# Optimization experiments

Measured on AMD Instinct MI355X. Metric: run time of the kernel, lower is better.

The kernel has to match this reference:

```python
import math
import jax, jax.numpy as jnp
import numpy as np

N_HEADS = 16
HIDDEN = 1024
FACTOR = 256
N_DK = HIDDEN // N_HEADS
B, S = 4, 2048


def _linear_params(key, fan_in, fan_out):
    kw, kb = jax.random.split(key)
    bound = 1.0 / math.sqrt(fan_in)
    W = jax.random.uniform(kw, (fan_in, fan_out), jnp.float32, -bound, bound)
    b = jax.random.uniform(kb, (fan_out,), jnp.float32, -bound, bound)
    return W, b


def setup_inputs() -> dict:
    key = jax.random.key(0)
    ks = jax.random.split(key, 12)
    inp = {
        "query": jax.random.normal(ks[0], (B, S, HIDDEN), jnp.float32),
        "key": jax.random.normal(ks[1], (B, S, HIDDEN), jnp.float32),
        "value": jax.random.normal(ks[2], (B, S, HIDDEN), jnp.float32),
        "mask": jax.random.randint(ks[3], (B, S), 0, 2, jnp.int32),
    }
    names = [("pq", HIDDEN, FACTOR), ("tq", FACTOR, HIDDEN),
             ("pk", HIDDEN, FACTOR), ("tk", FACTOR, HIDDEN),
             ("pv", HIDDEN, FACTOR), ("tv", FACTOR, HIDDEN),
             ("po", HIDDEN, FACTOR), ("to", FACTOR, HIDDEN)]
    for i, (nm, fi, fo) in enumerate(names):
        W, b = _linear_params(ks[4 + i], fi, fo)
        inp[f"W{nm}"], inp[f"b{nm}"] = W, b
    return inp


def _factored(x, Wp, bp, Wt, bt):
    # proj -> leaky_relu(0.2) -> tran
    h = jax.nn.leaky_relu(x @ Wp + bp, negative_slope=0.2)
    return h @ Wt + bt


def reference(query, key, value, mask,
              Wpq, bpq, Wtq, btq, Wpk, bpk, Wtk, btk,
              Wpv, bpv, Wtv, btv, Wpo, bpo, Wto, bto):
    bsize = query.shape[0]

    def split_heads(x):  # [B,S,H*Dk] -> [B,H,S,Dk]
        return x.reshape(bsize, -1, N_HEADS, N_DK).transpose(0, 2, 1, 3)

    q = split_heads(_factored(query, Wpq, bpq, Wtq, btq))
    k = split_heads(_factored(key, Wpk, bpk, Wtk, btk))
    v = split_heads(_factored(value, Wpv, bpv, Wtv, btv))

    scores = jnp.einsum("bhqd,bhkd->bhqk", q, k) / math.sqrt(N_DK)
    m = (mask == 0)[:, None, None, :]  # [B,1,1,S]
    scores = jnp.where(m, jnp.float32(-1e20), scores)
    attn = jax.nn.softmax(scores, axis=-1)
    cv = jnp.einsum("bhqk,bhkd->bhqd", attn, v)
    cv = cv.transpose(0, 2, 1, 3).reshape(bsize, -1, N_HEADS * N_DK)
    # dropout omitted (eval mode / deterministic reference)
    return _factored(cv, Wpo, bpo, Wto, bto)
```

## Files before the change

### kernel.cpp

```cpp
#include <hip/hip_runtime.h>
#include <cstdint>
#include <cstddef>

typedef __bf16 bf16_t;
typedef __bf16 bf16x8 __attribute__((ext_vector_type(8)));
typedef float  f32x4  __attribute__((ext_vector_type(4)));
typedef unsigned int uint32x4 __attribute__((ext_vector_type(4)));
typedef unsigned int uint32x2 __attribute__((ext_vector_type(2)));

#define DEV_INLINE __device__ __forceinline__

constexpr int Bsz = 4, Ssz = 2048, HID = 1024, FAC = 256, NH = 16, DKc = 64;
constexpr int Mrows = Bsz * Ssz;
constexpr float QSCALE = 0.18033688011112042f;

struct Ptr8 { const float* p[8]; };
struct Ptr3 { const float* p[3]; };

DEV_INLINE float fast_exp2(float x) {
#if __has_builtin(__builtin_amdgcn_exp2f)
  return __builtin_amdgcn_exp2f(x);
#else
  return exp2f(x);
#endif
}

DEV_INLINE void async16(const void* g, void* l) {
  __builtin_amdgcn_global_load_lds((const __attribute__((address_space(1))) void*)g,
                                   (__attribute__((address_space(3))) void*)l, 16, 0, 0);
}

#define WBAR(N) do { \
  asm volatile("s_waitcnt vmcnt(" #N ") lgkmcnt(0)" ::: "memory"); \
  __builtin_amdgcn_s_barrier(); \
} while (0)

DEV_INLINE int SW(int r) { return (r & 3) | ((r >> 1) & 4); }

__global__ __launch_bounds__(256) void k_prep(Ptr8 w, Ptr8 bsrc, const int* __restrict__ mask,
                                              bf16_t* wpt, bf16_t* wtt,
                                              float* bp, float* bt, float* mf, bf16_t* mb) {
  const int z = blockIdx.z;
  if (z == 8) {
    const int bid = blockIdx.y * 32 + blockIdx.x;
    if (bid >= 64) return;
    const int i = bid * 256 + threadIdx.x;
    if (i < 4 * FAC) bp[i] = bsrc.p[i >> 8][i & 255];
    if (i < 4 * HID) bt[i] = bsrc.p[4 + (i >> 10)][i & 1023];
    if (i < Bsz * Ssz) {
      const float m = (mask[i] != 0) ? 1.f : 0.f;
      mf[i] = m;
      mb[i] = (bf16_t)m;
    }
    return;
  }
  const int K = (z < 4) ? HID : FAC;
  const int N = (z < 4) ? FAC : HID;
  if ((int)(blockIdx.x * 32) >= N || (int)(blockIdx.y * 32) >= K) return;
  __shared__ float t[32][33];
  const float* src = w.p[z];
  bf16_t* dst = (z < 4) ? (wpt + (size_t)z * FAC * HID) : (wtt + (size_t)(z - 4) * FAC * HID);
  const int tx = threadIdx.x & 31, ty = threadIdx.x >> 5;
  const int kb = blockIdx.y * 32, nb = blockIdx.x * 32;
#pragma unroll
  for (int j = 0; j < 4; ++j)
    t[ty + j * 8][tx] = src[(size_t)(kb + ty + j * 8) * N + nb + tx];
  __syncthreads();
#pragma unroll
  for (int j = 0; j < 4; ++j)
    dst[(size_t)(nb + ty + j * 8) * K + kb + tx] = (bf16_t)t[tx][ty + j * 8];
}

__global__ __launch_bounds__(256, 3) void k_gemmP2(Ptr3 Asrc,
                                                   const bf16_t* __restrict__ Bt_,
                                                   const float* __restrict__ biasAll,
                                                   bf16_t* __restrict__ Call) {
  __shared__ __align__(16) bf16_t As[3][64 * 40];
  __shared__ __align__(16) bf16_t Bs[4][128 * 32];

  const int z = blockIdx.z;
  const bf16_t* Bt = Bt_ + (size_t)z * FAC * HID;
  const float* bias = biasAll + z * FAC;
  bf16_t* C = Call + (size_t)z * Mrows * FAC;

  const int tid = threadIdx.x;
  const int lane = tid & 63, wave = tid >> 6;
  const int quad = lane >> 4, l16 = lane & 15;
  const int m0 = blockIdx.y * 64, n0 = blockIdx.x * 128;

  const int brow = wave * 16 + (lane >> 2), bkc = (lane & 3) * 8;
  const bf16_t* gB0 = Bt + (size_t)(n0 + brow) * HID + bkc;
  const bf16_t* gB1 = gB0 + (size_t)64 * HID;

  const int crow = tid >> 2, chalf = (tid & 3) * 8;
  const float* gAf = Asrc.p[z] + (size_t)(m0 + crow) * HID + chalf;

#define ASYNCB(t, buf)                                \
  do {                                                \
    const int k0_ = (t) * 32;                         \
    async16(gB0 + k0_, Bs[buf] + wave * 512);         \
    async16(gB1 + k0_, Bs[buf] + 2048 + wave * 512);  \
  } while (0)

  {
    f32x4 pa = *(const f32x4*)gAf;
    f32x4 pb = *(const f32x4*)(gAf + 4);
    __builtin_amdgcn_sched_barrier(0);
    ASYNCB(0, 0);
    ASYNCB(1, 1);
    union { bf16_t h[8]; uint32x4 u; } o;
#pragma unroll
    for (int j = 0; j < 4; ++j) { o.h[j] = (bf16_t)pa[j]; o.h[4 + j] = (bf16_t)pb[j]; }
    *(uint32x4*)(As[0] + crow * 40 + chalf) = o.u;
  }

  f32x4 acc[4][2] = {};
  constexpr int nk = 32;

  for (int it = 0; it < nk; ++it) {
    f32x4 xa, xb;
    const int k1 = (it + 1) * 32;
    if (it + 1 < nk) {
      xa = *(const f32x4*)(gAf + k1);
      xb = *(const f32x4*)(gAf + k1 + 4);
    }
    __builtin_amdgcn_sched_barrier(0);
    if (it + 2 < nk) ASYNCB(it + 2, (it + 2) & 3);

    if (it + 2 < nk)      WBAR(6);
    else if (it + 1 < nk) WBAR(4);
    else                  WBAR(0);

    const bf16_t* Ac = As[it % 3];
    const bf16_t* Bc = Bs[it & 3];
    bf16x8 af[4], bfr[2];
#pragma unroll
    for (int i = 0; i < 4; ++i)
      af[i] = *(const bf16x8*)(Ac + (i * 16 + l16) * 40 + quad * 8);
#pragma unroll
    for (int i = 0; i < 2; ++i)
      bfr[i] = *(const bf16x8*)(Bc + (wave * 32 + i * 16 + l16) * 32 + quad * 8);
#pragma unroll
    for (int mi = 0; mi < 4; ++mi)
#pragma unroll
      for (int ni = 0; ni < 2; ++ni)
        acc[mi][ni] = __builtin_amdgcn_mfma_f32_16x16x32_bf16(af[mi], bfr[ni], acc[mi][ni], 0, 0, 0);

    if (it + 1 < nk) {
      union { bf16_t h[8]; uint32x4 u; } o;
#pragma unroll
      for (int j = 0; j < 4; ++j) { o.h[j] = (bf16_t)xa[j]; o.h[4 + j] = (bf16_t)xb[j]; }
      *(uint32x4*)(As[(it + 1) % 3] + crow * 40 + chalf) = o.u;
    }
  }
#undef ASYNCB

#pragma unroll
  for (int mi = 0; mi < 4; ++mi) {
    const int rbase = m0 + mi * 16 + quad * 4;
#pragma unroll
    for (int ni = 0; ni < 2; ++ni) {
      const int col = n0 + wave * 32 + ni * 16 + l16;
      const float bv = bias[col];
#pragma unroll
      for (int r = 0; r < 4; ++r) {
        float y = acc[mi][ni][r] + bv;
        y = (y > 0.f) ? y : 0.2f * y;
        C[(size_t)(rbase + r) * FAC + col] = (bf16_t)y;
      }
    }
  }
}

template <int EPI, typename OUT_T>
__global__ __launch_bounds__(256, 2) void k_gemmQ(const bf16_t* __restrict__ Aall,
                                                  const bf16_t* __restrict__ Btall,
                                                  const float* __restrict__ biasAll,
                                                  OUT_T* __restrict__ Call,
                                                  bf16_t* __restrict__ C2,
                                                  const float* __restrict__ rowmul,
                                                  int N, int K,
                                                  long long Az, long long Bz, long long Cz, int biasz) {
  __shared__ __align__(16) bf16_t As[5][128 * 32];
  __shared__ __align__(16) bf16_t Bs[5][128 * 32];

  const int z = blockIdx.z;
  const bf16_t* Bt = Btall + (size_t)z * Bz;
  const float* bias = biasAll + (size_t)z * biasz;
  OUT_T* C = Call + (size_t)z * Cz;

  const int tid = threadIdx.x;
  const int lane = tid & 63, wave = tid >> 6;
  const int quad = lane >> 4, l16 = lane & 15;
  const int wr = wave >> 1, wc = wave & 1;
  const int m0 = blockIdx.y * 128, n0 = blockIdx.x * 128;

  const int arow = wave * 16 + (lane >> 2), akc = (lane & 3) * 8;
  const bf16_t* gB0 = Bt + (size_t)(n0 + arow) * K + akc;
  const bf16_t* gB1 = gB0 + (size_t)64 * K;
  const bf16_t* A = Aall + (size_t)z * Az;
  const bf16_t* gA0 = A + (size_t)(m0 + arow) * K + akc;
  const bf16_t* gA1 = gA0 + (size_t)64 * K;

#define STAGEQ(t, buf)                               \
  do {                                               \
    const int k0_ = (t) * 32;                        \
    async16(gA0 + k0_, As[buf] + wave * 512);        \
    async16(gA1 + k0_, As[buf] + 2048 + wave * 512); \
    async16(gB0 + k0_, Bs[buf] + wave * 512);        \
    async16(gB1 + k0_, Bs[buf] + 2048 + wave * 512); \
  } while (0)

  const int nk = K / 32;
  STAGEQ(0, 0);
  STAGEQ(1, 1);
  STAGEQ(2, 2);

  f32x4 acc[4][4] = {};

  for (int it = 0; it < nk; ++it) {
    if (it + 3 < nk) STAGEQ(it + 3, (it + 3) % 5);

    if (it + 3 < nk)      WBAR(12);
    else if (it + 2 < nk) WBAR(8);
    else if (it + 1 < nk) WBAR(4);
    else                  WBAR(0);

    const bf16_t* Ac = As[it % 5];
    const bf16_t* Bc = Bs[it % 5];
    bf16x8 af[4], bfr[4];
#pragma unroll
    for (int i = 0; i < 4; ++i)
      af[i] = *(const bf16x8*)(Ac + (wr * 64 + i * 16 + l16) * 32 + quad * 8);
#pragma unroll
    for (int i = 0; i < 4; ++i)
      bfr[i] = *(const bf16x8*)(Bc + (wc * 64 + i * 16 + l16) * 32 + quad * 8);
#pragma unroll
    for (int mi = 0; mi < 4; ++mi)
#pragma unroll
      for (int ni = 0; ni < 4; ++ni)
        acc[mi][ni] = __builtin_amdgcn_mfma_f32_16x16x32_bf16(af[mi], bfr[ni], acc[mi][ni], 0, 0, 0);
  }
#undef STAGEQ

  if (EPI == 1 && z == 2) {
#pragma unroll
    for (int mi = 0; mi < 4; ++mi) {
      const int rbase = m0 + wr * 64 + mi * 16 + quad * 4;
      const int bb = rbase >> 11, s = rbase & 2047;
      float rmv[4];
#pragma unroll
      for (int r = 0; r < 4; ++r) rmv[r] = rowmul[rbase + r];
#pragma unroll
      for (int ni = 0; ni < 4; ++ni) {
        const int col = n0 + wc * 64 + ni * 16 + l16;
        const float bv = bias[col];
        const int hh = col >> 6, d = col & 63;
        union { bf16_t e[4]; uint32x2 u; } p;
#pragma unroll
        for (int r = 0; r < 4; ++r) p.e[r] = (bf16_t)((acc[mi][ni][r] + bv) * rmv[r]);
        *(uint32x2*)(C2 + (((size_t)((bb * NH + hh) * DKc + d)) << 11) + s) = p.u;
      }
    }
    return;
  }

  const float scale = (EPI == 1 && z == 0) ? QSCALE : 1.f;
#pragma unroll
  for (int mi = 0; mi < 4; ++mi) {
    const int rbase = m0 + wr * 64 + mi * 16 + quad * 4;
#pragma unroll
    for (int ni = 0; ni < 4; ++ni) {
      const int col = n0 + wc * 64 + ni * 16 + l16;
      const float bv = bias[col];
#pragma unroll
      for (int r = 0; r < 4; ++r) {
        float y = (acc[mi][ni][r] + bv) * scale;
        C[(size_t)(rbase + r) * N + col] = (OUT_T)y;
      }
    }
  }
}

__global__ __launch_bounds__(128, 2) void k_gemmO(const bf16_t* __restrict__ A,
                                                  const bf16_t* __restrict__ Bt,
                                                  const float* __restrict__ bias,
                                                  bf16_t* __restrict__ C) {
  __shared__ __align__(16) bf16_t As[5][64 * 32];
  __shared__ __align__(16) bf16_t Bs[5][64 * 32];

  const int tid = threadIdx.x;
  const int lane = tid & 63, wave = tid >> 6;
  const int quad = lane >> 4, l16 = lane & 15;
  const int m0 = blockIdx.y * 64, n0 = blockIdx.x * 64;

  const int srow = wave * 32 + (lane >> 2), skc = (lane & 3) * 8;
  const bf16_t* gA0 = A + (size_t)(m0 + srow) * HID + skc;
  const bf16_t* gA1 = gA0 + (size_t)16 * HID;
  const bf16_t* gB0 = Bt + (size_t)(n0 + srow) * HID + skc;
  const bf16_t* gB1 = gB0 + (size_t)16 * HID;

#define STAGEO(t, buf)                                 \
  do {                                                 \
    const int k0_ = (t) * 32;                          \
    async16(gA0 + k0_, As[buf] + wave * 1024);         \
    async16(gA1 + k0_, As[buf] + wave * 1024 + 512);   \
    async16(gB0 + k0_, Bs[buf] + wave * 1024);         \
    async16(gB1 + k0_, Bs[buf] + wave * 1024 + 512);   \
  } while (0)

  constexpr int nk = HID / 32;
  STAGEO(0, 0);
  STAGEO(1, 1);
  STAGEO(2, 2);

  f32x4 acc[4][2] = {};

  for (int it = 0; it < nk; ++it) {
    if (it + 3 < nk) STAGEO(it + 3, (it + 3) % 5);

    if (it + 3 < nk)      WBAR(12);
    else if (it + 2 < nk) WBAR(8);
    else if (it + 1 < nk) WBAR(4);
    else                  WBAR(0);

    const bf16_t* Ac = As[it % 5];
    const bf16_t* Bc = Bs[it % 5];
    bf16x8 af[4], bfr[2];
#pragma unroll
    for (int i = 0; i < 4; ++i)
      af[i] = *(const bf16x8*)(Ac + (i * 16 + l16) * 32 + quad * 8);
#pragma unroll
    for (int i = 0; i < 2; ++i)
      bfr[i] = *(const bf16x8*)(Bc + (wave * 32 + i * 16 + l16) * 32 + quad * 8);
#pragma unroll
    for (int mi = 0; mi < 4; ++mi)
#pragma unroll
      for (int ni = 0; ni < 2; ++ni)
        acc[mi][ni] = __builtin_amdgcn_mfma_f32_16x16x32_bf16(af[mi], bfr[ni], acc[mi][ni], 0, 0, 0);
  }
#undef STAGEO

#pragma unroll
  for (int mi = 0; mi < 4; ++mi) {
    const int rbase = m0 + mi * 16 + quad * 4;
#pragma unroll
    for (int ni = 0; ni < 2; ++ni) {
      const int col = n0 + wave * 32 + ni * 16 + l16;
      const float bv = bias[col];
#pragma unroll
      for (int r = 0; r < 4; ++r) {
        float y = acc[mi][ni][r] + bv;
        y = (y > 0.f) ? y : 0.2f * y;
        C[(size_t)(rbase + r) * FAC + col] = (bf16_t)y;
      }
    }
  }
}

__global__ __launch_bounds__(512, 2) void k_attn(const bf16_t* __restrict__ qkv,
                                                 const bf16_t* __restrict__ mb,
                                                 bf16_t* __restrict__ cv) {
  __shared__ __align__(16) bf16_t Ks[4][64 * 64];
  __shared__ __align__(16) bf16_t Vt[4][64 * 64];
  __shared__ __align__(16) bf16_t Ml[Ssz];

  const int qt = blockIdx.x, h = blockIdx.y, b = blockIdx.z;
  const bf16_t* qp = qkv;
  const bf16_t* kp = qkv + (size_t)Mrows * HID;
  const bf16_t* vtp = qkv + 2 * (size_t)Mrows * HID + (size_t)(b * NH + h) * DKc * Ssz;

  const int tid = threadIdx.x;
  const int lane = tid & 63, wave = tid >> 6;
  const int quad = lane >> 4, l16 = lane & 15;

  const int r0 = wave * 8 + (lane >> 3);
  const int c0 = ((lane & 7) ^ SW(r0)) * 8;
  const int ldsOff = wave * 512;
  const bf16_t* kgA = kp + (size_t)(b * Ssz + r0) * HID + h * DKc + c0;
  const bf16_t* vgA = vtp + (size_t)r0 * Ssz + c0;

#define STAGEA(t, buf)                                          \
  do {                                                          \
    async16(kgA + (size_t)(t) * 64 * HID, Ks[buf] + ldsOff);    \
    async16(vgA + (t) * 64, Vt[buf] + ldsOff);                  \
  } while (0)

  *(uint32x2*)(Ml + tid * 4) = *(const uint32x2*)(mb + (size_t)b * Ssz + tid * 4);
  STAGEA(0, 0);
  STAGEA(1, 1);

  bf16x8 aq0[4], aq1[4];
#pragma unroll
  for (int g = 0; g < 4; ++g) {
    const size_t qrow = (size_t)(b * Ssz + qt * 512 + g * 128 + wave * 16 + l16) * HID + h * DKc + quad * 8;
    aq0[g] = *(const bf16x8*)(qp + qrow);
    aq1[g] = *(const bf16x8*)(qp + qrow + 32);
  }

  const int krow = 8 * (l16 >> 2) + (l16 & 3);
  f32x4 acc[4][4] = {};
  f32x4 dacc[4] = {};
  const bf16x8 zfrag = {};

  for (int kt = 0; kt < 32; ++kt) {
    if (kt + 2 < 32) STAGEA(kt + 2, (kt + 2) & 3);

    if (kt + 2 < 32)      WBAR(4);
    else if (kt + 1 < 32) WBAR(2);
    else                  WBAR(0);

    const bf16_t* Kc = Ks[kt & 3];
    const bf16_t* Vc = Vt[kt & 3];

    union U { uint32x4 u; bf16x8 h; } ap0[4], ap1[4];
    constexpr int koff[4] = {0, 4, 32, 36};
#pragma unroll
    for (int ks = 0; ks < 4; ++ks) {
      const int row = krow + koff[ks];
      const int sw = SW(row);
      bf16x8 a0 = *(const bf16x8*)(Kc + row * 64 + (quad ^ sw) * 8);
      bf16x8 a1 = *(const bf16x8*)(Kc + row * 64 + ((quad + 4) ^ sw) * 8);
#pragma unroll
      for (int g = 0; g < 4; ++g) {
        f32x4 c = {};
        c = __builtin_amdgcn_mfma_f32_16x16x32_bf16(a0, aq0[g], c, 0, 0, 0);
        c = __builtin_amdgcn_mfma_f32_16x16x32_bf16(a1, aq1[g], c, 0, 0, 0);
        union { bf16_t h[2]; uint32_t u; } p01, p23;
        p01.h[0] = (bf16_t)fast_exp2(c[0]);
        p01.h[1] = (bf16_t)fast_exp2(c[1]);
        p23.h[0] = (bf16_t)fast_exp2(c[2]);
        p23.h[1] = (bf16_t)fast_exp2(c[3]);
        U& t = (ks < 2) ? ap0[g] : ap1[g];
        t.u[(ks & 1) * 2] = p01.u;
        t.u[(ks & 1) * 2 + 1] = p23.u;
      }
    }

    bf16x8 mr0 = *(const bf16x8*)(Ml + kt * 64 + quad * 8);
    bf16x8 mr1 = *(const bf16x8*)(Ml + kt * 64 + 32 + quad * 8);
    if (l16 != 0) { mr0 = zfrag; mr1 = zfrag; }

    __builtin_amdgcn_s_setprio(1);
#pragma unroll
    for (int g = 0; g < 4; ++g) {
      dacc[g] = __builtin_amdgcn_mfma_f32_16x16x32_bf16(ap0[g].h, mr0, dacc[g], 0, 0, 0);
      dacc[g] = __builtin_amdgcn_mfma_f32_16x16x32_bf16(ap1[g].h, mr1, dacc[g], 0, 0, 0);
    }

#pragma unroll
    for (int d = 0; d < 4; ++d) {
      const int row = d * 16 + l16;
      const int sw = SW(row);
      bf16x8 bv0 = *(const bf16x8*)(Vc + row * 64 + (quad ^ sw) * 8);
      bf16x8 bv1 = *(const bf16x8*)(Vc + row * 64 + ((quad + 4) ^ sw) * 8);
#pragma unroll
      for (int g = 0; g < 4; ++g) {
        acc[g][d] = __builtin_amdgcn_mfma_f32_16x16x32_bf16(ap0[g].h, bv0, acc[g][d], 0, 0, 0);
        acc[g][d] = __builtin_amdgcn_mfma_f32_16x16x32_bf16(ap1[g].h, bv1, acc[g][d], 0, 0, 0);
      }
    }
    __builtin_amdgcn_s_setprio(0);
  }
#undef STAGEA

#pragma unroll
  for (int g = 0; g < 4; ++g) {
    const size_t obase = (size_t)(b * Ssz + qt * 512 + g * 128 + wave * 16 + quad * 4) * HID + h * DKc + l16;
#pragma unroll
    for (int r = 0; r < 4; ++r) {
      const float denom = __shfl(dacc[g][r], lane & 48, 64);
      const float rl = 1.f / denom;
#pragma unroll
      for (int d = 0; d < 4; ++d)
        cv[obase + (size_t)r * HID + d * 16] = (bf16_t)(acc[g][d][r] * rl);
    }
  }
}

extern "C" void kernel_launch(void* const* d_in, const int* in_sizes, int n_in,
                              void* d_out, int out_size, void* d_ws, size_t ws_size,
                              hipStream_t stream) {
  (void)in_sizes; (void)n_in; (void)out_size; (void)ws_size;
  const float* q_in = (const float*)d_in[0];
  const float* k_in = (const float*)d_in[1];
  const float* v_in = (const float*)d_in[2];
  const int* mask = (const int*)d_in[3];

  bf16_t* XB = (bf16_t*)d_ws;
  bf16_t* H3 = XB + (size_t)3 * Mrows * HID;
  bf16_t* CV = H3 + (size_t)3 * Mrows * FAC;
  bf16_t* WPT = CV + (size_t)Mrows * HID;
  bf16_t* WTT = WPT + (size_t)4 * FAC * HID;
  float* BP = (float*)(WTT + (size_t)4 * FAC * HID);
  float* BT = BP + 4 * FAC;
  float* MF = BT + 4 * HID;
  bf16_t* MB = (bf16_t*)(MF + Mrows);
  bf16_t* VTg = XB + 2 * (size_t)Mrows * HID;

  Ptr8 w;
  w.p[0] = (const float*)d_in[4];  w.p[1] = (const float*)d_in[8];
  w.p[2] = (const float*)d_in[12]; w.p[3] = (const float*)d_in[16];
  w.p[4] = (const float*)d_in[6];  w.p[5] = (const float*)d_in[10];
  w.p[6] = (const float*)d_in[14]; w.p[7] = (const float*)d_in[18];
  Ptr8 bs;
  bs.p[0] = (const float*)d_in[5];  bs.p[1] = (const float*)d_in[9];
  bs.p[2] = (const float*)d_in[13]; bs.p[3] = (const float*)d_in[17];
  bs.p[4] = (const float*)d_in[7];  bs.p[5] = (const float*)d_in[11];
  bs.p[6] = (const float*)d_in[15]; bs.p[7] = (const float*)d_in[19];
  hipLaunchKernelGGL(k_prep, dim3(32, 32, 9), dim3(256), 0, stream, w, bs, mask,
                     WPT, WTT, BP, BT, MF, MB);

  Ptr3 xs; xs.p[0] = q_in; xs.p[1] = k_in; xs.p[2] = v_in;

  hipLaunchKernelGGL(k_gemmP2, dim3(2, Mrows / 64, 3), dim3(256), 0, stream,
                     xs, WPT, BP, H3);

  hipLaunchKernelGGL((k_gemmQ<1, bf16_t>), dim3(HID / 128, Mrows / 128, 3), dim3(256), 0, stream,
                     H3, WTT, BT, XB, VTg, MF,
                     HID, FAC, (long long)Mrows * FAC, (long long)FAC * HID, (long long)Mrows * HID, HID);

  hipLaunchKernelGGL(k_attn, dim3(Ssz / 512, NH, Bsz), dim3(512), 0, stream, XB, MB, CV);

  hipLaunchKernelGGL(k_gemmO, dim3(FAC / 64, Mrows / 64, 1), dim3(128), 0, stream,
                     CV, WPT + (size_t)3 * FAC * HID, BP + 3 * FAC, H3);

  hipLaunchKernelGGL((k_gemmQ<2, float>), dim3(HID / 128, Mrows / 128, 1), dim3(256), 0, stream,
                     H3, WTT + (size_t)3 * FAC * HID, BT + 3 * HID, (float*)d_out, (bf16_t*)nullptr,
                     (const float*)nullptr, HID, FAC, 0LL, 0LL, 0LL, 0);
}
```

Before: 339.9 us.

## Compact prep grid, widen output-proj GEMM to four waves, drop attention setprio

The weight-transpose prep kernel now uses a 1D grid of exactly the tiles it needs, where before it launched a 32x32 grid per weight and returned early from most blocks. The output projection GEMM moves from 2 waves to 4 waves per 64x64 tile, each wave owning 16 rows, so there are fewer async loads and MFMAs per wave and more parallelism per CU. The s_setprio calls around the attention MFMA section are removed. Together these aim to cut idle launch overhead and raise occupancy, at the cost of less register-level reuse in the GEMM and possibly worse wave scheduling in attention.

```diff
diff --git a/kernel.cpp b/kernel.cpp
--- a/kernel.cpp
+++ b/kernel.cpp
@@ -42,9 +42,8 @@
                                               float* bp, float* bt, float* mf, bf16_t* mb) {
   const int z = blockIdx.z;
   if (z == 8) {
-    const int bid = blockIdx.y * 32 + blockIdx.x;
-    if (bid >= 64) return;
-    const int i = bid * 256 + threadIdx.x;
+    if (blockIdx.x >= 64) return;
+    const int i = blockIdx.x * 256 + threadIdx.x;
     if (i < 4 * FAC) bp[i] = bsrc.p[i >> 8][i & 255];
     if (i < 4 * HID) bt[i] = bsrc.p[4 + (i >> 10)][i & 1023];
     if (i < Bsz * Ssz) {
@@ -56,12 +55,12 @@
   }
   const int K = (z < 4) ? HID : FAC;
   const int N = (z < 4) ? FAC : HID;
-  if ((int)(blockIdx.x * 32) >= N || (int)(blockIdx.y * 32) >= K) return;
+  const int nbN = N / 32;
+  const int nb = (blockIdx.x % nbN) * 32, kb = (blockIdx.x / nbN) * 32;
   __shared__ float t[32][33];
   const float* src = w.p[z];
   bf16_t* dst = (z < 4) ? (wpt + (size_t)z * FAC * HID) : (wtt + (size_t)(z - 4) * FAC * HID);
   const int tx = threadIdx.x & 31, ty = threadIdx.x >> 5;
-  const int kb = blockIdx.y * 32, nb = blockIdx.x * 32;
 #pragma unroll
   for (int j = 0; j < 4; ++j)
     t[ty + j * 8][tx] = src[(size_t)(kb + ty + j * 8) * N + nb + tx];
@@ -282,7 +281,7 @@
   }
 }
 
-__global__ __launch_bounds__(128, 2) void k_gemmO(const bf16_t* __restrict__ A,
+__global__ __launch_bounds__(256, 2) void k_gemmO(const bf16_t* __restrict__ A,
                                                   const bf16_t* __restrict__ Bt,
                                                   const float* __restrict__ bias,
                                                   bf16_t* __restrict__ C) {
@@ -294,19 +293,15 @@
   const int quad = lane >> 4, l16 = lane & 15;
   const int m0 = blockIdx.y * 64, n0 = blockIdx.x * 64;
 
-  const int srow = wave * 32 + (lane >> 2), skc = (lane & 3) * 8;
+  const int srow = wave * 16 + (lane >> 2), skc = (lane & 3) * 8;
   const bf16_t* gA0 = A + (size_t)(m0 + srow) * HID + skc;
-  const bf16_t* gA1 = gA0 + (size_t)16 * HID;
   const bf16_t* gB0 = Bt + (size_t)(n0 + srow) * HID + skc;
-  const bf16_t* gB1 = gB0 + (size_t)16 * HID;
 
 #define STAGEO(t, buf)                                 \
   do {                                                 \
     const int k0_ = (t) * 32;                          \
-    async16(gA0 + k0_, As[buf] + wave * 1024);         \
-    async16(gA1 + k0_, As[buf] + wave * 1024 + 512);   \
-    async16(gB0 + k0_, Bs[buf] + wave * 1024);         \
-    async16(gB1 + k0_, Bs[buf] + wave * 1024 + 512);   \
+    async16(gA0 + k0_, As[buf] + wave * 512);          \
+    async16(gB0 + k0_, Bs[buf] + wave * 512);          \
   } while (0)
 
   constexpr int nk = HID / 32;
@@ -314,46 +309,39 @@
   STAGEO(1, 1);
   STAGEO(2, 2);
 
-  f32x4 acc[4][2] = {};
+  f32x4 acc[4] = {};
 
   for (int it = 0; it < nk; ++it) {
     if (it + 3 < nk) STAGEO(it + 3, (it + 3) % 5);
 
-    if (it + 3 < nk)      WBAR(12);
-    else if (it + 2 < nk) WBAR(8);
-    else if (it + 1 < nk) WBAR(4);
+    if (it + 3 < nk)      WBAR(6);
+    else if (it + 2 < nk) WBAR(4);
+    else if (it + 1 < nk) WBAR(2);
     else                  WBAR(0);
 
     const bf16_t* Ac = As[it % 5];
     const bf16_t* Bc = Bs[it % 5];
-    bf16x8 af[4], bfr[2];
+    bf16x8 af = *(const bf16x8*)(Ac + (wave * 16 + l16) * 32 + quad * 8);
+    bf16x8 bfr[4];
 #pragma unroll
     for (int i = 0; i < 4; ++i)
-      af[i] = *(const bf16x8*)(Ac + (i * 16 + l16) * 32 + quad * 8);
-#pragma unroll
-    for (int i = 0; i < 2; ++i)
-      bfr[i] = *(const bf16x8*)(Bc + (wave * 32 + i * 16 + l16) * 32 + quad * 8);
-#pragma unroll
-    for (int mi = 0; mi < 4; ++mi)
-#pragma unroll
-      for (int ni = 0; ni < 2; ++ni)
-        acc[mi][ni] = __builtin_amdgcn_mfma_f32_16x16x32_bf16(af[mi], bfr[ni], acc[mi][ni], 0, 0, 0);
+      bfr[i] = *(const bf16x8*)(Bc + (i * 16 + l16) * 32 + quad * 8);
+#pragma unroll
+    for (int ni = 0; ni < 4; ++ni)
+      acc[ni] = __builtin_amdgcn_mfma_f32_16x16x32_bf16(af, bfr[ni], acc[ni], 0, 0, 0);
   }
 #undef STAGEO
 
-#pragma unroll
-  for (int mi = 0; mi < 4; ++mi) {
-    const int rbase = m0 + mi * 16 + quad * 4;
-#pragma unroll
-    for (int ni = 0; ni < 2; ++ni) {
-      const int col = n0 + wave * 32 + ni * 16 + l16;
-      const float bv = bias[col];
-#pragma unroll
-      for (int r = 0; r < 4; ++r) {
-        float y = acc[mi][ni][r] + bv;
-        y = (y > 0.f) ? y : 0.2f * y;
-        C[(size_t)(rbase + r) * FAC + col] = (bf16_t)y;
-      }
+  const int rbase = m0 + wave * 16 + quad * 4;
+#pragma unroll
+  for (int ni = 0; ni < 4; ++ni) {
+    const int col = n0 + ni * 16 + l16;
+    const float bv = bias[col];
+#pragma unroll
+    for (int r = 0; r < 4; ++r) {
+      float y = acc[ni][r] + bv;
+      y = (y > 0.f) ? y : 0.2f * y;
+      C[(size_t)(rbase + r) * FAC + col] = (bf16_t)y;
     }
   }
 }
@@ -440,8 +428,6 @@
     bf16x8 mr0 = *(const bf16x8*)(Ml + kt * 64 + quad * 8);
     bf16x8 mr1 = *(const bf16x8*)(Ml + kt * 64 + 32 + quad * 8);
     if (l16 != 0) { mr0 = zfrag; mr1 = zfrag; }
-
-    __builtin_amdgcn_s_setprio(1);
 #pragma unroll
     for (int g = 0; g < 4; ++g) {
       dacc[g] = __builtin_amdgcn_mfma_f32_16x16x32_bf16(ap0[g].h, mr0, dacc[g], 0, 0, 0);
@@ -460,7 +446,6 @@
         acc[g][d] = __builtin_amdgcn_mfma_f32_16x16x32_bf16(ap1[g].h, bv1, acc[g][d], 0, 0, 0);
       }
     }
-    __builtin_amdgcn_s_setprio(0);
   }
 #undef STAGEA
 
@@ -508,7 +493,7 @@
   bs.p[2] = (const float*)d_in[13]; bs.p[3] = (const float*)d_in[17];
   bs.p[4] = (const float*)d_in[7];  bs.p[5] = (const float*)d_in[11];
   bs.p[6] = (const float*)d_in[15]; bs.p[7] = (const float*)d_in[19];
-  hipLaunchKernelGGL(k_prep, dim3(32, 32, 9), dim3(256), 0, stream, w, bs, mask,
+  hipLaunchKernelGGL(k_prep, dim3(256, 1, 9), dim3(256), 0, stream, w, bs, mask,
                      WPT, WTT, BP, BT, MF, MB);
 
   Ptr3 xs; xs.p[0] = q_in; xs.p[1] = k_in; xs.p[2] = v_in;
@@ -522,7 +507,7 @@
 
   hipLaunchKernelGGL(k_attn, dim3(Ssz / 512, NH, Bsz), dim3(512), 0, stream, XB, MB, CV);
 
-  hipLaunchKernelGGL(k_gemmO, dim3(FAC / 64, Mrows / 64, 1), dim3(128), 0, stream,
+  hipLaunchKernelGGL(k_gemmO, dim3(FAC / 64, Mrows / 64, 1), dim3(256), 0, stream,
                      CV, WPT + (size_t)3 * FAC * HID, BP + 3 * FAC, H3);
 
   hipLaunchKernelGGL((k_gemmQ<2, float>), dim3(HID / 128, Mrows / 128, 1), dim3(256), 0, stream,
```

Result: no change. 336.1 us (-1.1%).
